# Kernel optimization log

Hardware: AMD Instinct MI355X
Metric: run time of the kernel (lower is better)

The kernel has to match this reference:

```python
import jax, jax.numpy as jnp
import numpy as np

N, M, C, CSKIP, K = 16384, 4096, 256, 128, 3
BIG = 1e10  # distance penalty for cross-batch pairs


def setup_inputs() -> dict:
    key = jax.random.key(0)
    ks = jax.random.split(key, 6)
    return {
        "x": jax.random.normal(ks[0], (M, C), jnp.float32),
        "pos": jax.random.normal(ks[1], (M, 3), jnp.float32),
        "batch": jnp.zeros((M,), jnp.int32),
        "x_skip": jax.random.normal(ks[2], (N, CSKIP), jnp.float32),
        "pos_skip": jax.random.normal(ks[3], (N, 3), jnp.float32),
        "batch_skip": jnp.zeros((N,), jnp.int32),
        "W1": jax.random.normal(ks[4], (C + CSKIP, 256), jnp.float32) * (1.0 / np.sqrt(C + CSKIP)),
        "b1": jnp.zeros((256,), jnp.float32),
        "W2": jax.random.normal(ks[5], (256, 256), jnp.float32) * (1.0 / np.sqrt(256)),
        "b2": jnp.zeros((256,), jnp.float32),
    }


def _knn_idx(pos, pos_skip, batch, batch_skip, k):
    # Squared distances via GEMM form: [N, M]
    a2 = jnp.sum(pos_skip * pos_skip, axis=-1, keepdims=True)      # [N,1]
    b2 = jnp.sum(pos * pos, axis=-1)[None, :]                       # [1,M]
    d2 = a2 + b2 - 2.0 * (pos_skip @ pos.T)                         # [N,M]
    d2 = jnp.where(batch_skip[:, None] != batch[None, :], BIG, d2)
    _, idx = jax.lax.top_k(-d2, k)                                  # [N,k]
    return idx


def reference(x, pos, batch, x_skip, pos_skip, batch_skip, W1, b1, W2, b2):
    idx = _knn_idx(pos, pos_skip, batch, batch_skip, K)             # [N,k] coarse neighbor ids
    # Exact squared dist recomputed from gathered positions (matches torch diff path)
    diff = pos_skip[:, None, :] - pos[idx]                          # [N,k,3]
    d2 = jnp.sum(diff * diff, axis=-1, keepdims=True)               # [N,k,1]
    w = 1.0 / (d2 + 1e-8)                                           # inverse-distance weights
    wsum = jnp.sum(w, axis=1, keepdims=True)                        # per-row scatter_add == sum over k
    w = w / (wsum + 1e-8)
    x_interp = jnp.sum(w * x[idx], axis=1)                          # [N,C]
    h = jnp.concatenate([x_interp, x_skip], axis=1)                 # [N,C+C']
    h = jax.nn.relu(h @ W1 + b1)
    h = jax.nn.relu(h @ W2 + b2)
    return h
```

## Files before the change

kernel.cpp:

```cpp
#include <hip/hip_runtime.h>

typedef float     f4   __attribute__((ext_vector_type(4)));
typedef float     f32x4 __attribute__((ext_vector_type(4)));
typedef _Float16  h8   __attribute__((ext_vector_type(8)));
typedef _Float16  h4   __attribute__((ext_vector_type(4)));
typedef _Float16  h2   __attribute__((ext_vector_type(2)));

#define NQ   16384
#define MP   4096
#define CF   256
#define CSK  128
#define K1   384
#define HID  256
#define QB   16

__device__ __forceinline__ unsigned umed3(unsigned a, unsigned b, unsigned c) {
    unsigned r;
    asm("v_med3_u32 %0, %1, %2, %3" : "=v"(r) : "v"(a), "v"(b), "v"(c));
    return r;
}

__global__ __launch_bounds__(256) void wconv_kernel(
    const float* __restrict__ W1, const float* __restrict__ W2,
    _Float16* __restrict__ Wt1, _Float16* __restrict__ Wt2)
{
    const int i = blockIdx.x * 256 + threadIdx.x;
    if (i < K1 * HID) {
        const int k = i >> 8, n = i & 255;
        Wt1[(size_t)(k >> 5) * 8192 + ((k >> 3) & 3) * 2048 + n * 8 + (k & 7)]
            = (_Float16)W1[i];
    } else {
        const int i2 = i - K1 * HID;
        const int k = i2 >> 8, n = i2 & 255;
        Wt2[(size_t)(k >> 5) * 8192 + ((k >> 3) & 3) * 2048 + n * 8 + (k & 7)]
            = (_Float16)W2[i2];
    }
}

__global__ __launch_bounds__(256, 4) void fused_kernel(
    const float* __restrict__ pos,
    const float* __restrict__ pos_skip,
    const float* __restrict__ x,
    const float* __restrict__ x_skip,
    const _Float16* __restrict__ Wt1,
    const _Float16* __restrict__ Wt2,
    const float* __restrict__ b1,
    const float* __restrict__ b2,
    float* __restrict__ out)
{
    __shared__ __align__(16) char smem[26112];
    _Float16* pxh = (_Float16*)smem;
    _Float16* pyh = (_Float16*)(smem + 8192);
    _Float16* pzh = (_Float16*)(smem + 16384);
    unsigned short (*ci)[48] = (unsigned short (*)[48])(smem + 24576);
    int   (*fidx)[3] = (int (*)[3])(smem + 24576);
    float (*fw)[3]   = (float (*)[3])(smem + 24768);
    _Float16 (*As)[392] = (_Float16 (*)[392])smem;
    _Float16 (*Hs)[264] = (_Float16 (*)[264])smem;

    const int tid = threadIdx.x;

    {
        const f4* posv = (const f4*)pos;
        for (int m = tid; m < MP / 4; m += 256) {
            const f4 a = posv[3*m], b = posv[3*m+1], c = posv[3*m+2];
            h4 hx, hy, hz;
            hx[0]=(_Float16)a[0]; hx[1]=(_Float16)a[3];
            hx[2]=(_Float16)b[2]; hx[3]=(_Float16)c[1];
            hy[0]=(_Float16)a[1]; hy[1]=(_Float16)b[0];
            hy[2]=(_Float16)b[3]; hy[3]=(_Float16)c[2];
            hz[0]=(_Float16)a[2]; hz[1]=(_Float16)b[1];
            hz[2]=(_Float16)c[0]; hz[3]=(_Float16)c[3];
            *(h4*)&pxh[4*m] = hx;
            *(h4*)&pyh[4*m] = hy;
            *(h4*)&pzh[4*m] = hz;
        }
    }
    __syncthreads();

    const int lane = tid & 63;
    const int wv   = tid >> 6;

    {
        h2 q2x[4], q2y[4], q2z[4];
        #pragma unroll
        for (int k = 0; k < 4; k++) {
            const int q = blockIdx.x * QB + wv * 4 + k;
            const _Float16 hx = (_Float16)pos_skip[3*q+0];
            const _Float16 hy = (_Float16)pos_skip[3*q+1];
            const _Float16 hz = (_Float16)pos_skip[3*q+2];
            q2x[k][0] = hx; q2x[k][1] = hx;
            q2y[k][0] = hy; q2y[k][1] = hy;
            q2z[k][0] = hz; q2z[k][1] = hz;
        }

        unsigned K0[4], K1v[4], K2[4];
        #pragma unroll
        for (int k = 0; k < 4; k++) { K0[k] = ~0u; K1v[k] = ~0u; K2[k] = ~0u; }

        #define INS(k, key) {                                              \
            const unsigned o0 = K0[k], o1 = K1v[k], o2 = K2[k];            \
            K0[k]  = min(o0, (key));                                       \
            K1v[k] = umed3(o0, o1, (key));                                 \
            K2[k]  = umed3(o1, o2, (key));                                 \
        }

        union hpack { h4 v4; h2 v2[2]; };
        #define EVALP(CX, CY, CZ, JB)                                      \
            _Pragma("unroll")                                              \
            for (int k = 0; k < 4; k++) {                                  \
                _Pragma("unroll")                                          \
                for (int pp = 0; pp < 2; pp++) {                           \
                    const h2 dx = q2x[k] - (CX).v2[pp];                    \
                    const h2 dy = q2y[k] - (CY).v2[pp];                    \
                    const h2 dz = q2z[k] - (CZ).v2[pp];                    \
                    const h2 dd = dx*dx + dy*dy + dz*dz;                   \
                    const unsigned du = __builtin_bit_cast(unsigned, dd);  \
                    const unsigned key0 = ((du & 0xFFFFu) << 12) + (JB) + pp*2; \
                    const unsigned key1 = ((du >> 16) << 12) + (JB) + pp*2 + 1; \
                    INS(k, key0);                                          \
                    INS(k, key1);                                          \
                }                                                          \
            }

        const h4* px4 = (const h4*)pxh;
        const h4* py4 = (const h4*)pyh;
        const h4* pz4 = (const h4*)pzh;

        hpack cx, cy, cz, nx, ny, nz;
        int idx = lane;
        cx.v4 = px4[idx]; cy.v4 = py4[idx]; cz.v4 = pz4[idx];

        for (int it = 0; it < 16; ++it) {
            const int nidx = idx + 64;
            nx.v4 = px4[nidx]; ny.v4 = py4[nidx]; nz.v4 = pz4[nidx];
            const unsigned jb = (unsigned)(it * 256 + lane * 4);
            EVALP(cx, cy, cz, jb);
            cx = nx; cy = ny; cz = nz;
            idx = nidx;
        }
        #undef EVALP
        #undef INS

        #pragma unroll
        for (int k = 0; k < 4; k++) {
            unsigned a0 = K0[k], a1 = K1v[k], a2 = K2[k];
            {
                const unsigned b0 = (unsigned)__builtin_amdgcn_ds_swizzle((int)a0, 0x041F);
                const unsigned b1 = (unsigned)__builtin_amdgcn_ds_swizzle((int)a1, 0x041F);
                const unsigned b2 = (unsigned)__builtin_amdgcn_ds_swizzle((int)a2, 0x041F);
                const unsigned m0 = min(a0, b0);
                const unsigned c1 = max(a0, b0);
                const unsigned d0 = min(a1, b1), d1 = max(a1, b1);
                const unsigned m1 = min(c1, d0);
                const unsigned m2 = min(min(max(c1, d0), d1), min(a2, b2));
                a0 = m0; a1 = m1; a2 = m2;
            }
            {
                const unsigned b0 = (unsigned)__builtin_amdgcn_ds_swizzle((int)a0, 0x081F);
                const unsigned b1 = (unsigned)__builtin_amdgcn_ds_swizzle((int)a1, 0x081F);
                const unsigned b2 = (unsigned)__builtin_amdgcn_ds_swizzle((int)a2, 0x081F);
                const unsigned m0 = min(a0, b0);
                const unsigned c1 = max(a0, b0);
                const unsigned d0 = min(a1, b1), d1 = max(a1, b1);
                const unsigned m1 = min(c1, d0);
                const unsigned m2 = min(min(max(c1, d0), d1), min(a2, b2));
                a0 = m0; a1 = m1; a2 = m2;
            }
            if (!(lane & 3)) {
                const int q = wv * 4 + k;
                const int pr = lane >> 2;
                ci[q][pr*3+0] = (unsigned short)(a0 & 0xFFFu);
                ci[q][pr*3+1] = (unsigned short)(a1 & 0xFFFu);
                ci[q][pr*3+2] = (unsigned short)(a2 & 0xFFFu);
            }
        }
    }
    __syncthreads();

    if (tid < 8 * QB) {
        const int q    = tid >> 3;
        const int part = tid & 7;
        const int g    = blockIdx.x * QB + q;
        const double qxd = (double)pos_skip[3*g+0];
        const double qyd = (double)pos_skip[3*g+1];
        const double qzd = (double)pos_skip[3*g+2];
        const double a2d = qxd*qxd + qyd*qyd + qzd*qzd;

        double e0 = 1e300, e1 = 1e300, e2 = 1e300;
        int    j0 = 0,     j1 = 0,     j2 = 0;
        #pragma unroll
        for (int c = 0; c < 6; c++) {
            const int j = ci[q][part*6 + c];
            const double pxd = (double)pos[3*j+0];
            const double pyd = (double)pos[3*j+1];
            const double pzd = (double)pos[3*j+2];
            const double b2  = pxd*pxd + pyd*pyd + pzd*pzd;
            const double dot = qxd*pxd + qyd*pyd + qzd*pzd;
            const double d   = (a2d + b2) - 2.0 * dot;
            if (d < e2) {
                if (d < e1) {
                    e2 = e1; j2 = j1;
                    if (d < e0) { e1 = e0; j1 = j0; e0 = d; j0 = j; }
                    else        { e1 = d;  j1 = j; }
                } else { e2 = d; j2 = j; }
            }
        }
        ci[q][part*3+0] = (unsigned short)j0;
        ci[q][part*3+1] = (unsigned short)j1;
        ci[q][part*3+2] = (unsigned short)j2;
    }
    __syncthreads();

    if (tid < QB) {
        const int g = blockIdx.x * QB + tid;
        const double qxd = (double)pos_skip[3*g+0];
        const double qyd = (double)pos_skip[3*g+1];
        const double qzd = (double)pos_skip[3*g+2];
        const double a2d = qxd*qxd + qyd*qyd + qzd*qzd;

        double e0 = 1e300, e1 = 1e300, e2 = 1e300;
        int    j0 = 0,     j1 = 0,     j2 = 0;
        for (int p = 0; p < 8; p++) {
            #pragma unroll
            for (int s = 0; s < 3; s++) {
                const int j = ci[tid][p*3+s];
                const double pxd = (double)pos[3*j+0];
                const double pyd = (double)pos[3*j+1];
                const double pzd = (double)pos[3*j+2];
                const double b2  = pxd*pxd + pyd*pyd + pzd*pzd;
                const double dot = qxd*pxd + qyd*pyd + qzd*pzd;
                const double d   = (a2d + b2) - 2.0 * dot;
                if (d < e2) {
                    if (d < e1) {
                        e2 = e1; j2 = j1;
                        if (d < e0) { e1 = e0; j1 = j0; e0 = d; j0 = j; }
                        else        { e1 = d;  j1 = j; }
                    } else { e2 = d; j2 = j; }
                }
            }
        }
        const float sx = pos_skip[3*g+0], sy = pos_skip[3*g+1], sz = pos_skip[3*g+2];
        const int jj[3] = { j0, j1, j2 };
        float wv3[3];
        #pragma unroll
        for (int k = 0; k < 3; k++) {
            const float dx = sx - pos[3*jj[k]+0];
            const float dy = sy - pos[3*jj[k]+1];
            const float dz = sz - pos[3*jj[k]+2];
            const float dd = dx*dx + dy*dy + dz*dz;
            wv3[k] = 1.0f / (dd + 1e-8f);
        }
        const float inv = 1.0f / (wv3[0] + wv3[1] + wv3[2] + 1e-8f);
        #pragma unroll
        for (int k = 0; k < 3; k++) {
            fidx[tid][k] = jj[k];
            fw[tid][k]   = wv3[k] * inv;
        }
    }
    __syncthreads();

    const int row0 = blockIdx.x * QB;

    {
        const int r   = tid >> 4;
        const int sub = tid & 15;
        const int j0 = fidx[r][0], j1 = fidx[r][1], j2 = fidx[r][2];
        const float w0 = fw[r][0], w1 = fw[r][1], w2 = fw[r][2];
        const f4* xa = (const f4*)(x + (size_t)j0 * CF);
        const f4* xb = (const f4*)(x + (size_t)j1 * CF);
        const f4* xc = (const f4*)(x + (size_t)j2 * CF);
        const f4* xs = (const f4*)(x_skip + (size_t)(row0 + r) * CSK);
        #pragma unroll
        for (int t = 0; t < 4; t++) {
            const int c4 = t * 16 + sub;
            const f4 a = xa[c4], b = xb[c4], c = xc[c4];
            const f4 v = a * w0 + b * w1 + c * w2;
            h4 hv; hv[0]=(_Float16)v[0]; hv[1]=(_Float16)v[1];
                   hv[2]=(_Float16)v[2]; hv[3]=(_Float16)v[3];
            *(h4*)&As[r][c4 * 4] = hv;
        }
        #pragma unroll
        for (int t = 0; t < 2; t++) {
            const int c4 = t * 16 + sub;
            const f4 v = xs[c4];
            h4 hv; hv[0]=(_Float16)v[0]; hv[1]=(_Float16)v[1];
                   hv[2]=(_Float16)v[2]; hv[3]=(_Float16)v[3];
            *(h4*)&As[r][CF + c4 * 4] = hv;
        }
    }

    const int ln   = tid & 15;
    const int quad = (tid >> 4) & 3;
    const int nb   = wv * 64;
    const int q8   = quad * 8;

    const _Float16* w1b = Wt1 + quad * 2048 + (size_t)(nb + ln) * 8;
    const _Float16* w2b = Wt2 + quad * 2048 + (size_t)(nb + ln) * 8;

    f32x4 acc[4];
    #pragma unroll
    for (int nt = 0; nt < 4; nt++) acc[nt] = (f32x4)0.0f;

    h8 B[6][4];
    #pragma unroll
    for (int s = 0; s < 6; s++)
        #pragma unroll
        for (int nt = 0; nt < 4; nt++)
            B[s][nt] = *(const h8*)(w1b + (size_t)s * 8192 + nt * 128);

    __syncthreads();

    #pragma unroll
    for (int kb = 0; kb < 12; kb++) {
        const int s = kb % 6;
        const h8 ha = *(const h8*)&As[ln][kb*32 + q8];
        h8 hb[4];
        #pragma unroll
        for (int nt = 0; nt < 4; nt++) hb[nt] = B[s][nt];
        if (kb < 6) {
            #pragma unroll
            for (int nt = 0; nt < 4; nt++)
                B[s][nt] = *(const h8*)(w1b + (size_t)(kb+6) * 8192 + nt * 128);
        } else {
            #pragma unroll
            for (int nt = 0; nt < 4; nt++)
                B[s][nt] = *(const h8*)(w2b + (size_t)(kb-6) * 8192 + nt * 128);
        }
        #pragma unroll
        for (int nt = 0; nt < 4; nt++)
            acc[nt] = __builtin_amdgcn_mfma_f32_16x16x32_f16(ha, hb[nt], acc[nt], 0, 0, 0);
    }
    __syncthreads();

    #pragma unroll
    for (int nt = 0; nt < 4; nt++) {
        const int n = nb + nt*16 + ln;
        const float bv = b1[n];
        #pragma unroll
        for (int r = 0; r < 4; r++) {
            const int m = quad*4 + r;
            Hs[m][n] = (_Float16)fmaxf(acc[nt][r] + bv, 0.0f);
        }
        acc[nt] = (f32x4)0.0f;
    }
    __syncthreads();

    #pragma unroll
    for (int kb = 0; kb < 8; kb++) {
        const int s = kb % 6;
        const h8 ha = *(const h8*)&Hs[ln][kb*32 + q8];
        h8 hb[4];
        #pragma unroll
        for (int nt = 0; nt < 4; nt++) hb[nt] = B[s][nt];
        if (kb < 2) {
            #pragma unroll
            for (int nt = 0; nt < 4; nt++)
                B[s][nt] = *(const h8*)(w2b + (size_t)(kb+6) * 8192 + nt * 128);
        }
        #pragma unroll
        for (int nt = 0; nt < 4; nt++)
            acc[nt] = __builtin_amdgcn_mfma_f32_16x16x32_f16(ha, hb[nt], acc[nt], 0, 0, 0);
    }

    #pragma unroll
    for (int nt = 0; nt < 4; nt++) {
        const int n = nb + nt*16 + ln;
        const float bv = b2[n];
        #pragma unroll
        for (int r = 0; r < 4; r++) {
            const int m = quad*4 + r;
            out[(size_t)(row0 + m) * HID + n] = fmaxf(acc[nt][r] + bv, 0.0f);
        }
    }
}

extern "C" void kernel_launch(void* const* d_in, const int* in_sizes, int n_in,
                              void* d_out, int out_size, void* d_ws, size_t ws_size,
                              hipStream_t stream) {
    const float* x         = (const float*)d_in[0];
    const float* pos       = (const float*)d_in[1];
    const float* x_skip    = (const float*)d_in[3];
    const float* pos_skip  = (const float*)d_in[4];
    const float* W1        = (const float*)d_in[6];
    const float* b1        = (const float*)d_in[7];
    const float* W2        = (const float*)d_in[8];
    const float* b2        = (const float*)d_in[9];
    float* out = (float*)d_out;

    char* ws = (char*)d_ws;
    _Float16* Wt1 = (_Float16*)ws;
    _Float16* Wt2 = (_Float16*)(ws + 196608);

    wconv_kernel<<<(K1*HID + HID*HID) / 256, 256, 0, stream>>>(W1, W2, Wt1, Wt2);
    fused_kernel<<<NQ / QB, 256, 0, stream>>>(pos, pos_skip, x, x_skip,
                                              Wt1, Wt2, b1, b2, out);
}
```

Measured before the change: 117.3 us.

## Split fused kernel into KNN and MLP kernels with 64-row MLP tiles

Splits the single fused kernel into a KNN kernel, which writes neighbor indices and weights to workspace, and a separate MLP kernel. The MLP kernel handles 64 rows per block instead of 16, so each weight fragment loaded from global memory is reused across four row groups of MFMAs, cutting weight traffic per row by four. The cost is an extra launch, a global round-trip for the indices and weights, more accumulator registers, and twice the shared memory per block with lower occupancy.

```diff
diff --git a/kernel.cpp b/kernel.cpp
--- a/kernel.cpp
+++ b/kernel.cpp
@@ -13,6 +13,7 @@
 #define K1   384
 #define HID  256
 #define QB   16
+#define MB   64
 
 __device__ __forceinline__ unsigned umed3(unsigned a, unsigned b, unsigned c) {
     unsigned r;
@@ -37,26 +38,17 @@
     }
 }
 
-__global__ __launch_bounds__(256, 4) void fused_kernel(
+__global__ __launch_bounds__(256, 4) void knn_kernel(
     const float* __restrict__ pos,
     const float* __restrict__ pos_skip,
-    const float* __restrict__ x,
-    const float* __restrict__ x_skip,
-    const _Float16* __restrict__ Wt1,
-    const _Float16* __restrict__ Wt2,
-    const float* __restrict__ b1,
-    const float* __restrict__ b2,
-    float* __restrict__ out)
+    unsigned short* __restrict__ fidx_g,
+    float* __restrict__ fw_g)
 {
     __shared__ __align__(16) char smem[26112];
     _Float16* pxh = (_Float16*)smem;
     _Float16* pyh = (_Float16*)(smem + 8192);
     _Float16* pzh = (_Float16*)(smem + 16384);
     unsigned short (*ci)[48] = (unsigned short (*)[48])(smem + 24576);
-    int   (*fidx)[3] = (int (*)[3])(smem + 24576);
-    float (*fw)[3]   = (float (*)[3])(smem + 24768);
-    _Float16 (*As)[392] = (_Float16 (*)[392])smem;
-    _Float16 (*Hs)[264] = (_Float16 (*)[264])smem;
 
     const int tid = threadIdx.x;
 
@@ -254,26 +246,43 @@
         const float inv = 1.0f / (wv3[0] + wv3[1] + wv3[2] + 1e-8f);
         #pragma unroll
         for (int k = 0; k < 3; k++) {
-            fidx[tid][k] = jj[k];
-            fw[tid][k]   = wv3[k] * inv;
-        }
-    }
-    __syncthreads();
-
-    const int row0 = blockIdx.x * QB;
+            fidx_g[g*3+k] = (unsigned short)jj[k];
+            fw_g[g*3+k]   = wv3[k] * inv;
+        }
+    }
+}
+
+__global__ __launch_bounds__(256, 2) void mlp_kernel(
+    const float* __restrict__ x,
+    const float* __restrict__ x_skip,
+    const _Float16* __restrict__ Wt1,
+    const _Float16* __restrict__ Wt2,
+    const float* __restrict__ b1,
+    const float* __restrict__ b2,
+    const unsigned short* __restrict__ fidx_g,
+    const float* __restrict__ fw_g,
+    float* __restrict__ out)
+{
+    __shared__ __align__(16) char smem[50176];
+    _Float16 (*As)[392] = (_Float16 (*)[392])smem;
+    _Float16 (*Hs)[264] = (_Float16 (*)[264])smem;
+
+    const int tid  = threadIdx.x;
+    const int row0 = blockIdx.x * MB;
 
     {
-        const int r   = tid >> 4;
-        const int sub = tid & 15;
-        const int j0 = fidx[r][0], j1 = fidx[r][1], j2 = fidx[r][2];
-        const float w0 = fw[r][0], w1 = fw[r][1], w2 = fw[r][2];
+        const int r   = tid >> 2;
+        const int sub = tid & 3;
+        const int g   = row0 + r;
+        const int j0 = fidx_g[g*3+0], j1 = fidx_g[g*3+1], j2 = fidx_g[g*3+2];
+        const float w0 = fw_g[g*3+0], w1 = fw_g[g*3+1], w2 = fw_g[g*3+2];
         const f4* xa = (const f4*)(x + (size_t)j0 * CF);
         const f4* xb = (const f4*)(x + (size_t)j1 * CF);
         const f4* xc = (const f4*)(x + (size_t)j2 * CF);
-        const f4* xs = (const f4*)(x_skip + (size_t)(row0 + r) * CSK);
-        #pragma unroll
-        for (int t = 0; t < 4; t++) {
-            const int c4 = t * 16 + sub;
+        const f4* xs = (const f4*)(x_skip + (size_t)g * CSK);
+        #pragma unroll
+        for (int t = 0; t < 16; t++) {
+            const int c4 = t * 4 + sub;
             const f4 a = xa[c4], b = xb[c4], c = xc[c4];
             const f4 v = a * w0 + b * w1 + c * w2;
             h4 hv; hv[0]=(_Float16)v[0]; hv[1]=(_Float16)v[1];
@@ -281,8 +290,8 @@
             *(h4*)&As[r][c4 * 4] = hv;
         }
         #pragma unroll
-        for (int t = 0; t < 2; t++) {
-            const int c4 = t * 16 + sub;
+        for (int t = 0; t < 8; t++) {
+            const int c4 = t * 4 + sub;
             const f4 v = xs[c4];
             h4 hv; hv[0]=(_Float16)v[0]; hv[1]=(_Float16)v[1];
                    hv[2]=(_Float16)v[2]; hv[3]=(_Float16)v[3];
@@ -292,19 +301,22 @@
 
     const int ln   = tid & 15;
     const int quad = (tid >> 4) & 3;
+    const int wv   = tid >> 6;
     const int nb   = wv * 64;
     const int q8   = quad * 8;
 
     const _Float16* w1b = Wt1 + quad * 2048 + (size_t)(nb + ln) * 8;
     const _Float16* w2b = Wt2 + quad * 2048 + (size_t)(nb + ln) * 8;
 
-    f32x4 acc[4];
-    #pragma unroll
-    for (int nt = 0; nt < 4; nt++) acc[nt] = (f32x4)0.0f;
-
-    h8 B[6][4];
-    #pragma unroll
-    for (int s = 0; s < 6; s++)
+    f32x4 acc[4][4];
+    #pragma unroll
+    for (int rg = 0; rg < 4; rg++)
+        #pragma unroll
+        for (int nt = 0; nt < 4; nt++) acc[rg][nt] = (f32x4)0.0f;
+
+    h8 B[2][4];
+    #pragma unroll
+    for (int s = 0; s < 2; s++)
         #pragma unroll
         for (int nt = 0; nt < 4; nt++)
             B[s][nt] = *(const h8*)(w1b + (size_t)s * 8192 + nt * 128);
@@ -313,64 +325,78 @@
 
     #pragma unroll
     for (int kb = 0; kb < 12; kb++) {
-        const int s = kb % 6;
-        const h8 ha = *(const h8*)&As[ln][kb*32 + q8];
+        const int s = kb & 1;
         h8 hb[4];
         #pragma unroll
         for (int nt = 0; nt < 4; nt++) hb[nt] = B[s][nt];
-        if (kb < 6) {
+        const int nk = kb + 2;
+        if (nk < 12) {
             #pragma unroll
             for (int nt = 0; nt < 4; nt++)
-                B[s][nt] = *(const h8*)(w1b + (size_t)(kb+6) * 8192 + nt * 128);
+                B[s][nt] = *(const h8*)(w1b + (size_t)nk * 8192 + nt * 128);
         } else {
             #pragma unroll
             for (int nt = 0; nt < 4; nt++)
-                B[s][nt] = *(const h8*)(w2b + (size_t)(kb-6) * 8192 + nt * 128);
-        }
-        #pragma unroll
-        for (int nt = 0; nt < 4; nt++)
-            acc[nt] = __builtin_amdgcn_mfma_f32_16x16x32_f16(ha, hb[nt], acc[nt], 0, 0, 0);
+                B[s][nt] = *(const h8*)(w2b + (size_t)(nk - 12) * 8192 + nt * 128);
+        }
+        #pragma unroll
+        for (int rg = 0; rg < 4; rg++) {
+            const h8 ha = *(const h8*)&As[rg * 16 + ln][kb * 32 + q8];
+            #pragma unroll
+            for (int nt = 0; nt < 4; nt++)
+                acc[rg][nt] = __builtin_amdgcn_mfma_f32_16x16x32_f16(ha, hb[nt], acc[rg][nt], 0, 0, 0);
+        }
     }
     __syncthreads();
 
     #pragma unroll
     for (int nt = 0; nt < 4; nt++) {
-        const int n = nb + nt*16 + ln;
+        const int n = nb + nt * 16 + ln;
         const float bv = b1[n];
         #pragma unroll
-        for (int r = 0; r < 4; r++) {
-            const int m = quad*4 + r;
-            Hs[m][n] = (_Float16)fmaxf(acc[nt][r] + bv, 0.0f);
-        }
-        acc[nt] = (f32x4)0.0f;
+        for (int rg = 0; rg < 4; rg++) {
+            #pragma unroll
+            for (int r = 0; r < 4; r++) {
+                Hs[rg * 16 + quad * 4 + r][n] =
+                    (_Float16)fmaxf(acc[rg][nt][r] + bv, 0.0f);
+            }
+            acc[rg][nt] = (f32x4)0.0f;
+        }
     }
     __syncthreads();
 
     #pragma unroll
     for (int kb = 0; kb < 8; kb++) {
-        const int s = kb % 6;
-        const h8 ha = *(const h8*)&Hs[ln][kb*32 + q8];
+        const int s = kb & 1;
         h8 hb[4];
         #pragma unroll
         for (int nt = 0; nt < 4; nt++) hb[nt] = B[s][nt];
-        if (kb < 2) {
+        const int nk = kb + 2;
+        if (nk < 8) {
             #pragma unroll
             for (int nt = 0; nt < 4; nt++)
-                B[s][nt] = *(const h8*)(w2b + (size_t)(kb+6) * 8192 + nt * 128);
-        }
-        #pragma unroll
-        for (int nt = 0; nt < 4; nt++)
-            acc[nt] = __builtin_amdgcn_mfma_f32_16x16x32_f16(ha, hb[nt], acc[nt], 0, 0, 0);
+                B[s][nt] = *(const h8*)(w2b + (size_t)nk * 8192 + nt * 128);
+        }
+        #pragma unroll
+        for (int rg = 0; rg < 4; rg++) {
+            const h8 ha = *(const h8*)&Hs[rg * 16 + ln][kb * 32 + q8];
+            #pragma unroll
+            for (int nt = 0; nt < 4; nt++)
+                acc[rg][nt] = __builtin_amdgcn_mfma_f32_16x16x32_f16(ha, hb[nt], acc[rg][nt], 0, 0, 0);
+        }
     }
 
     #pragma unroll
     for (int nt = 0; nt < 4; nt++) {
-        const int n = nb + nt*16 + ln;
+        const int n = nb + nt * 16 + ln;
         const float bv = b2[n];
         #pragma unroll
-        for (int r = 0; r < 4; r++) {
-            const int m = quad*4 + r;
-            out[(size_t)(row0 + m) * HID + n] = fmaxf(acc[nt][r] + bv, 0.0f);
+        for (int rg = 0; rg < 4; rg++) {
+            #pragma unroll
+            for (int r = 0; r < 4; r++) {
+                const int m = rg * 16 + quad * 4 + r;
+                out[(size_t)(row0 + m) * HID + n] = fmaxf(acc[rg][nt][r] + bv, 0.0f);
+            }
         }
     }
 }
@@ -389,10 +415,13 @@
     float* out = (float*)d_out;
 
     char* ws = (char*)d_ws;
-    _Float16* Wt1 = (_Float16*)ws;
-    _Float16* Wt2 = (_Float16*)(ws + 196608);
+    _Float16*       Wt1    = (_Float16*)ws;
+    _Float16*       Wt2    = (_Float16*)(ws + 196608);
+    unsigned short* fidx_g = (unsigned short*)(ws + 327680);
+    float*          fw_g   = (float*)(ws + 425984);
 
     wconv_kernel<<<(K1*HID + HID*HID) / 256, 256, 0, stream>>>(W1, W2, Wt1, Wt2);
-    fused_kernel<<<NQ / QB, 256, 0, stream>>>(pos, pos_skip, x, x_skip,
-                                              Wt1, Wt2, b1, b2, out);
+    knn_kernel<<<NQ / QB, 256, 0, stream>>>(pos, pos_skip, fidx_g, fw_g);
+    mlp_kernel<<<NQ / MB, 256, 0, stream>>>(x, x_skip, Wt1, Wt2, b1, b2,
+                                            fidx_g, fw_g, out);
 }
```

Measured after the change: 126.8 us. 1.08x slower.
